# Kernel tuning notes

Hardware: AMD Instinct MI355X
Metric: run time of the kernel (lower is better)

## Reference

```python
import jax, jax.numpy as jnp
import numpy as np
from jax import lax

B = 65536
N_STEPS = 256
WHEELBASE = 2.7
DT = 0.05
MAX_STEER = float(np.deg2rad(30.0))
MAX_SPEED = 100.0
FRICTION_ROAD = 0.1
FRICTION_AIR = 0.01


def setup_inputs() -> dict:
    key = jax.random.key(0)
    k1, k2, k3, k4, k5, k6 = jax.random.split(key, 6)
    return {
        "start_x": jax.random.normal(k1, (B,), dtype=jnp.float32),
        "start_y": jax.random.normal(k2, (B,), dtype=jnp.float32),
        "start_yaw": jax.random.normal(k3, (B,), dtype=jnp.float32),
        "start_speed": jax.random.uniform(k4, (B,), dtype=jnp.float32) * 20.0,
        "accel": jax.random.normal(k5, (B, N_STEPS), dtype=jnp.float32),
        "steering": jax.random.normal(k6, (B, N_STEPS), dtype=jnp.float32),
    }


def reference(start_x, start_y, start_yaw, start_speed, accel, steering):
    # One scan step = one iteration of the original python loop, vectorized over B.
    def step(carry, ctrl):
        x, y, yaw, sp = carry
        a, st = ctrl
        friction = sp * FRICTION_ROAD + FRICTION_AIR * sp * sp
        sp_next = jnp.clip(sp + DT * (a - friction), 0.0, MAX_SPEED)
        steer = jnp.clip(st, -MAX_STEER, MAX_STEER)
        ang_vel = sp * jnp.tan(steer) / WHEELBASE
        x_next = x + sp * jnp.cos(yaw) * DT
        y_next = y + sp * jnp.sin(yaw) * DT
        yaw_next = yaw + ang_vel * DT
        new = (x_next, y_next, yaw_next, sp_next)
        return new, new

    # Controls for steps 0..n_steps-2 (last control unused, as in the original loop).
    ctrls = (accel[:, : N_STEPS - 1].T, steering[:, : N_STEPS - 1].T)  # [T-1, B]
    init = (start_x, start_y, start_yaw, start_speed)
    _, traj = lax.scan(step, init, ctrls)  # each leaf [T-1, B]

    def full(s0, rest):
        return jnp.concatenate([s0[None, :], rest], axis=0).T  # [B, T]

    x = full(start_x, traj[0])
    y = full(start_y, traj[1])
    yaw = full(start_yaw, traj[2])
    speed = full(start_speed, traj[3])
    return (x, y, yaw, speed)
```

## Files before the change

kernel.cpp:

```cpp
#include <hip/hip_runtime.h>

#define T 256
#define TC 16
#define SC 32
#define V 128
#define DT 0.05f
#define WHEELBASE 2.7f
#define MAX_STEER 0.5235987755982988f
#define MAX_SPEED 100.0f
#define FR 0.1f
#define FA 0.01f

__global__ __launch_bounds__(V) void bicycle_kernel(
    const float* __restrict__ sx, const float* __restrict__ sy,
    const float* __restrict__ syaw, const float* __restrict__ ssp,
    const float* __restrict__ accel, const float* __restrict__ steering,
    float* __restrict__ out, int B)
{
    __shared__ float lds[4][V][TC + 1];

    const int tid = threadIdx.x;
    const int b   = blockIdx.x * V + tid;

    float x   = sx[b];
    float y   = sy[b];
    float yaw = syaw[b];
    float sp  = ssp[b];

    const float4* a4 = (const float4*)(accel    + (size_t)b * T);
    const float4* s4 = (const float4*)(steering + (size_t)b * T);

    const size_t plane   = (size_t)B * T;
    const size_t vehBase = (size_t)blockIdx.x * V;

    for (int c = 0; c < T / SC; ++c) {
        float4 av[SC / 4], sv[SC / 4];
        #pragma unroll
        for (int i = 0; i < SC / 4; ++i) {
            av[i] = a4[c * (SC / 4) + i];
            sv[i] = s4[c * (SC / 4) + i];
        }
        float ac[SC], sc[SC];
        #pragma unroll
        for (int i = 0; i < SC / 4; ++i) {
            ac[4*i+0] = av[i].x; ac[4*i+1] = av[i].y; ac[4*i+2] = av[i].z; ac[4*i+3] = av[i].w;
            sc[4*i+0] = sv[i].x; sc[4*i+1] = sv[i].y; sc[4*i+2] = sv[i].z; sc[4*i+3] = sv[i].w;
        }

        #pragma unroll
        for (int h = 0; h < 2; ++h) {
            #pragma unroll
            for (int j = 0; j < TC; ++j) {
                const int t = h * TC + j;
                lds[0][tid][j] = x;
                lds[1][tid][j] = y;
                lds[2][tid][j] = yaw;
                lds[3][tid][j] = sp;

                float fr    = fmaf(FA * sp, sp, sp * FR);
                float spn   = fmaf(DT, ac[t] - fr, sp);
                spn         = fminf(fmaxf(spn, 0.0f), MAX_SPEED);
                float steer = fminf(fmaxf(sc[t], -MAX_STEER), MAX_STEER);
                float angv  = sp * __tanf(steer) * (1.0f / WHEELBASE);
                float s_, c_;
                __sincosf(yaw, &s_, &c_);
                float spDT = sp * DT;
                x   = fmaf(spDT, c_, x);
                y   = fmaf(spDT, s_, y);
                yaw = fmaf(angv, DT, yaw);
                sp  = spn;
            }
            __syncthreads();

            const int t0 = c * SC + h * TC;
            #pragma unroll
            for (int p = 0; p < 4; ++p) {
                float* op = out + (size_t)p * plane + vehBase * T + t0;
                #pragma unroll
                for (int i = 0; i < TC; ++i) {
                    const int n  = i * V + tid;
                    const int vv = n >> 4;
                    const int j  = n & 15;
                    op[(size_t)vv * T + j] = lds[p][vv][j];
                }
            }
            __syncthreads();
        }
    }
}

extern "C" void kernel_launch(void* const* d_in, const int* in_sizes, int n_in,
                              void* d_out, int out_size, void* d_ws, size_t ws_size,
                              hipStream_t stream) {
    const float* sx       = (const float*)d_in[0];
    const float* sy       = (const float*)d_in[1];
    const float* syaw     = (const float*)d_in[2];
    const float* ssp      = (const float*)d_in[3];
    const float* accel    = (const float*)d_in[4];
    const float* steering = (const float*)d_in[5];
    float* out = (float*)d_out;

    int B = in_sizes[0];
    dim3 block(V);
    dim3 grid(B / V);
    hipLaunchKernelGGL(bicycle_kernel, grid, block, 0, stream,
                       sx, sy, syaw, ssp, accel, steering, out, B);
}
```

Before: 431.5 us.

## Use single-wave blocks with LDS waitcnt fences, prefetch controls, nontemporal stores

```diff
diff --git a/kernel.cpp b/kernel.cpp
--- a/kernel.cpp
+++ b/kernel.cpp
@@ -3,7 +3,8 @@
 #define T 256
 #define TC 16
 #define SC 32
-#define V 128
+#define NSC (T / SC)
+#define V 64
 #define DT 0.05f
 #define WHEELBASE 2.7f
 #define MAX_STEER 0.5235987755982988f
@@ -11,13 +12,17 @@
 #define FR 0.1f
 #define FA 0.01f
 
+__device__ __forceinline__ void lds_fence() {
+    asm volatile("s_waitcnt lgkmcnt(0)" ::: "memory");
+}
+
 __global__ __launch_bounds__(V) void bicycle_kernel(
     const float* __restrict__ sx, const float* __restrict__ sy,
     const float* __restrict__ syaw, const float* __restrict__ ssp,
     const float* __restrict__ accel, const float* __restrict__ steering,
     float* __restrict__ out, int B)
 {
-    __shared__ float lds[4][V][TC + 1];
+    __shared__ float lds[2][4][V][TC + 1];
 
     const int tid = threadIdx.x;
     const int b   = blockIdx.x * V + tid;
@@ -33,34 +38,45 @@
     const size_t plane   = (size_t)B * T;
     const size_t vehBase = (size_t)blockIdx.x * V;
 
-    for (int c = 0; c < T / SC; ++c) {
-        float4 av[SC / 4], sv[SC / 4];
+    const int u = tid >> 4;
+    const int j = tid & 15;
+
+    float4 av[SC / 4], sv[SC / 4], avn[SC / 4], svn[SC / 4];
+    #pragma unroll
+    for (int i = 0; i < SC / 4; ++i) { av[i] = a4[i]; sv[i] = s4[i]; }
+
+    for (int c = 0; c < NSC; ++c) {
+        if (c + 1 < NSC) {
+            #pragma unroll
+            for (int i = 0; i < SC / 4; ++i) {
+                avn[i] = a4[(c + 1) * (SC / 4) + i];
+                svn[i] = s4[(c + 1) * (SC / 4) + i];
+            }
+        }
+
+        float ac[SC], scn[SC];
         #pragma unroll
         for (int i = 0; i < SC / 4; ++i) {
-            av[i] = a4[c * (SC / 4) + i];
-            sv[i] = s4[c * (SC / 4) + i];
-        }
-        float ac[SC], sc[SC];
-        #pragma unroll
-        for (int i = 0; i < SC / 4; ++i) {
-            ac[4*i+0] = av[i].x; ac[4*i+1] = av[i].y; ac[4*i+2] = av[i].z; ac[4*i+3] = av[i].w;
-            sc[4*i+0] = sv[i].x; sc[4*i+1] = sv[i].y; sc[4*i+2] = sv[i].z; sc[4*i+3] = sv[i].w;
+            ac[4*i+0]  = av[i].x; ac[4*i+1]  = av[i].y; ac[4*i+2]  = av[i].z; ac[4*i+3]  = av[i].w;
+            scn[4*i+0] = sv[i].x; scn[4*i+1] = sv[i].y; scn[4*i+2] = sv[i].z; scn[4*i+3] = sv[i].w;
         }
 
         #pragma unroll
         for (int h = 0; h < 2; ++h) {
+            const int buf = h;
+
             #pragma unroll
-            for (int j = 0; j < TC; ++j) {
-                const int t = h * TC + j;
-                lds[0][tid][j] = x;
-                lds[1][tid][j] = y;
-                lds[2][tid][j] = yaw;
-                lds[3][tid][j] = sp;
+            for (int jj = 0; jj < TC; ++jj) {
+                const int t = h * TC + jj;
+                lds[buf][0][tid][jj] = x;
+                lds[buf][1][tid][jj] = y;
+                lds[buf][2][tid][jj] = yaw;
+                lds[buf][3][tid][jj] = sp;
 
                 float fr    = fmaf(FA * sp, sp, sp * FR);
                 float spn   = fmaf(DT, ac[t] - fr, sp);
                 spn         = fminf(fmaxf(spn, 0.0f), MAX_SPEED);
-                float steer = fminf(fmaxf(sc[t], -MAX_STEER), MAX_STEER);
+                float steer = fminf(fmaxf(scn[t], -MAX_STEER), MAX_STEER);
                 float angv  = sp * __tanf(steer) * (1.0f / WHEELBASE);
                 float s_, c_;
                 __sincosf(yaw, &s_, &c_);
@@ -70,7 +86,8 @@
                 yaw = fmaf(angv, DT, yaw);
                 sp  = spn;
             }
-            __syncthreads();
+
+            lds_fence();
 
             const int t0 = c * SC + h * TC;
             #pragma unroll
@@ -78,13 +95,16 @@
                 float* op = out + (size_t)p * plane + vehBase * T + t0;
                 #pragma unroll
                 for (int i = 0; i < TC; ++i) {
-                    const int n  = i * V + tid;
-                    const int vv = n >> 4;
-                    const int j  = n & 15;
-                    op[(size_t)vv * T + j] = lds[p][vv][j];
+                    const int vv = i * 4 + u;
+                    __builtin_nontemporal_store(lds[buf][p][vv][j],
+                                                &op[(size_t)vv * T + j]);
                 }
             }
-            __syncthreads();
+        }
+
+        if (c + 1 < NSC) {
+            #pragma unroll
+            for (int i = 0; i < SC / 4; ++i) { av[i] = avn[i]; sv[i] = svn[i]; }
         }
     }
 }
@@ -96,8 +116,8 @@
     const float* sy       = (const float*)d_in[1];
     const float* syaw     = (const float*)d_in[2];
     const float* ssp      = (const float*)d_in[3];
+    const float* steering = (const float*)d_in[5];
     const float* accel    = (const float*)d_in[4];
-    const float* steering = (const float*)d_in[5];
     float* out = (float*)d_out;
 
     int B = in_sizes[0];
```

After: 413.3 us. 1.04x faster.

## Use single-wave blocks with wave barriers and double-buffered control prefetch

Applied to the files above, without the earlier changes.

```diff
diff --git a/kernel.cpp b/kernel.cpp
--- a/kernel.cpp
+++ b/kernel.cpp
@@ -2,8 +2,8 @@
 
 #define T 256
 #define TC 16
-#define SC 32
-#define V 128
+#define NC (T / TC)
+#define V 64
 #define DT 0.05f
 #define WHEELBASE 2.7f
 #define MAX_STEER 0.5235987755982988f
@@ -11,7 +11,7 @@
 #define FR 0.1f
 #define FA 0.01f
 
-__global__ __launch_bounds__(V) void bicycle_kernel(
+__global__ __launch_bounds__(V, 3) void bicycle_kernel(
     const float* __restrict__ sx, const float* __restrict__ sy,
     const float* __restrict__ syaw, const float* __restrict__ ssp,
     const float* __restrict__ accel, const float* __restrict__ steering,
@@ -33,60 +33,69 @@
     const size_t plane   = (size_t)B * T;
     const size_t vehBase = (size_t)blockIdx.x * V;
 
-    for (int c = 0; c < T / SC; ++c) {
-        float4 av[SC / 4], sv[SC / 4];
-        #pragma unroll
-        for (int i = 0; i < SC / 4; ++i) {
-            av[i] = a4[c * (SC / 4) + i];
-            sv[i] = s4[c * (SC / 4) + i];
-        }
-        float ac[SC], sc[SC];
-        #pragma unroll
-        for (int i = 0; i < SC / 4; ++i) {
-            ac[4*i+0] = av[i].x; ac[4*i+1] = av[i].y; ac[4*i+2] = av[i].z; ac[4*i+3] = av[i].w;
-            sc[4*i+0] = sv[i].x; sc[4*i+1] = sv[i].y; sc[4*i+2] = sv[i].z; sc[4*i+3] = sv[i].w;
-        }
+    const int u = tid >> 4;
+    const int j = tid & 15;
 
-        #pragma unroll
-        for (int h = 0; h < 2; ++h) {
-            #pragma unroll
-            for (int j = 0; j < TC; ++j) {
-                const int t = h * TC + j;
-                lds[0][tid][j] = x;
-                lds[1][tid][j] = y;
-                lds[2][tid][j] = yaw;
-                lds[3][tid][j] = sp;
+    float4 avA[TC / 4], svA[TC / 4], avB[TC / 4], svB[TC / 4];
+    #pragma unroll
+    for (int i = 0; i < TC / 4; ++i) { avA[i] = a4[i]; svA[i] = s4[i]; }
 
-                float fr    = fmaf(FA * sp, sp, sp * FR);
-                float spn   = fmaf(DT, ac[t] - fr, sp);
-                spn         = fminf(fmaxf(spn, 0.0f), MAX_SPEED);
-                float steer = fminf(fmaxf(sc[t], -MAX_STEER), MAX_STEER);
-                float angv  = sp * __tanf(steer) * (1.0f / WHEELBASE);
-                float s_, c_;
-                __sincosf(yaw, &s_, &c_);
-                float spDT = sp * DT;
-                x   = fmaf(spDT, c_, x);
-                y   = fmaf(spDT, s_, y);
-                yaw = fmaf(angv, DT, yaw);
-                sp  = spn;
-            }
-            __syncthreads();
+#define CHUNK(C, AV, SV, AVN, SVN)                                         \
+  {                                                                        \
+    const int c_ = (C);                                                    \
+    if (c_ + 1 < NC) {                                                     \
+      _Pragma("unroll")                                                    \
+      for (int i = 0; i < TC / 4; ++i) {                                   \
+        AVN[i] = a4[(c_ + 1) * (TC / 4) + i];                              \
+        SVN[i] = s4[(c_ + 1) * (TC / 4) + i];                              \
+      }                                                                    \
+    }                                                                      \
+    _Pragma("unroll")                                                      \
+    for (int k = 0; k < TC / 4; ++k) {                                     \
+      const float acx[4] = {AV[k].x, AV[k].y, AV[k].z, AV[k].w};           \
+      const float scx[4] = {SV[k].x, SV[k].y, SV[k].z, SV[k].w};           \
+      _Pragma("unroll")                                                    \
+      for (int m = 0; m < 4; ++m) {                                        \
+        const int tt = k * 4 + m;                                          \
+        lds[0][tid][tt] = x;                                               \
+        lds[1][tid][tt] = y;                                               \
+        lds[2][tid][tt] = yaw;                                             \
+        lds[3][tid][tt] = sp;                                              \
+        float fr    = fmaf(FA * sp, sp, sp * FR);                          \
+        float spn   = fmaf(DT, acx[m] - fr, sp);                           \
+        spn         = fminf(fmaxf(spn, 0.0f), MAX_SPEED);                  \
+        float steer = fminf(fmaxf(scx[m], -MAX_STEER), MAX_STEER);         \
+        float angv  = sp * __tanf(steer) * (1.0f / WHEELBASE);             \
+        float s_, c2_;                                                     \
+        __sincosf(yaw, &s_, &c2_);                                         \
+        float spDT = sp * DT;                                              \
+        x   = fmaf(spDT, c2_, x);                                          \
+        y   = fmaf(spDT, s_, y);                                           \
+        yaw = fmaf(angv, DT, yaw);                                         \
+        sp  = spn;                                                         \
+      }                                                                    \
+    }                                                                      \
+    __builtin_amdgcn_wave_barrier();    \
+    {                                                                      \
+      const int t0 = c_ * TC;                                              \
+      _Pragma("unroll")                                                    \
+      for (int p = 0; p < 4; ++p) {                                        \
+        float* op = out + (size_t)p * plane + vehBase * T + t0;            \
+        _Pragma("unroll")                                                  \
+        for (int i = 0; i < TC; ++i) {                                     \
+          const int vv = i * 4 + u;                                        \
+          op[(size_t)vv * T + j] = lds[p][vv][j];                          \
+        }                                                                  \
+      }                                                                    \
+    }                                                                      \
+    __builtin_amdgcn_wave_barrier();     \
+  }
 
-            const int t0 = c * SC + h * TC;
-            #pragma unroll
-            for (int p = 0; p < 4; ++p) {
-                float* op = out + (size_t)p * plane + vehBase * T + t0;
-                #pragma unroll
-                for (int i = 0; i < TC; ++i) {
-                    const int n  = i * V + tid;
-                    const int vv = n >> 4;
-                    const int j  = n & 15;
-                    op[(size_t)vv * T + j] = lds[p][vv][j];
-                }
-            }
-            __syncthreads();
-        }
+    for (int c = 0; c < NC; c += 2) {
+        CHUNK(c,     avA, svA, avB, svB)
+        CHUNK(c + 1, avB, svB, avA, svA)
     }
+#undef CHUNK
 }
 
 extern "C" void kernel_launch(void* const* d_in, const int* in_sizes, int n_in,
```

New measurement: 503.4 us. +16.7%, slower.
